# Performance work log

Measured on AMD Instinct MI355X. Metric: run time of the kernel, lower is better.

Reference implementation:

```python
import jax, jax.numpy as jnp
import numpy as np

B, I, P, H = 256, 1024, 128, 128
L_PROT = 1024
ATOMS_PER_MOL = 128
N_LIG = B * ATOMS_PER_MOL  # 32768 total ligand atoms


def setup_inputs() -> dict:
    key = jax.random.key(0)
    ks = jax.random.split(key, 6)
    param_enc = jax.random.normal(ks[0], (B, I, P), dtype=jnp.float32)
    h_prot = jax.random.normal(ks[1], (B, L_PROT, H), dtype=jnp.float32)
    w1 = jax.random.normal(ks[2], (P, 1), dtype=jnp.float32) / np.sqrt(P)
    b1 = jax.random.normal(ks[3], (1,), dtype=jnp.float32)
    indices_lig = jax.random.randint(ks[4], (B, I), 0, ATOMS_PER_MOL)
    indices_prot = jax.random.randint(ks[5], (B, I), 0, L_PROT)
    protein_idx = jnp.arange(B)            # complex b -> protein row b
    lig_offsets = jnp.arange(B) * ATOMS_PER_MOL  # 'split' cumulative atom offsets
    mask = jnp.ones((B, I), dtype=bool)    # valid (non -510 padded) interactions
    return {
        "param_enc": param_enc, "h_prot": h_prot, "w1": w1, "b1": b1,
        "indices_lig": indices_lig, "indices_prot": indices_prot,
        "protein_idx": protein_idx, "lig_offsets": lig_offsets, "mask": mask,
    }


def reference(param_enc, h_prot, w1, b1, indices_lig, indices_prot,
              protein_idx, lig_offsets, mask):
    # scalar gate per interaction: ReLU(Linear(param_enc))  (dropout = identity, eval mode)
    gate = jax.nn.relu(jnp.einsum("bip,po->bio", param_enc, w1) + b1)  # [B, I, 1]
    # gather protein residue features: h_prot[protein_idx[b], indices_prot[b,i], :]
    gathered = h_prot[protein_idx[:, None], indices_prot]              # [B, I, H]
    contrib = gate * gathered * mask[..., None]                        # [B, I, H]
    # scatter-add into per-ligand-atom accumulator at split + i_l
    glob = (lig_offsets[:, None] + indices_lig).reshape(-1)            # [B*I]
    protein_inter = jnp.zeros((N_LIG, H), dtype=contrib.dtype)
    protein_inter = protein_inter.at[glob].add(contrib.reshape(-1, H))
    return protein_inter
```

## Files before the change

kernel.cpp:

```cpp
#include <hip/hip_runtime.h>

#define B_ 256
#define I_ 1024
#define P_ 128
#define H_ 128
#define LP_ 1024

__global__ __launch_bounds__(256) void gates_gemv(
    const float* __restrict__ param_enc,
    const float* __restrict__ w1,
    const float* __restrict__ b1,
    float* __restrict__ gates)
{
    const int tid  = threadIdx.x;
    const int lane = tid & 63;
    const int wave = tid >> 6;
    const int half = lane >> 5;
    const int sub  = lane & 31;
    const int w    = blockIdx.x * 4 + wave;
    const int b    = w >> 5;
    const int wwb  = w & 31;

    const float bias = b1[0];
    const float4 wv = *(const float4*)(w1 + sub * 4);
    const float* pe_b = param_enc + (size_t)b * I_ * P_;
    float* g_b = gates + b * I_;

    #pragma unroll 8
    for (int q = 0; q < 16; ++q) {
        const int i0 = (wwb + q * 32) * 2;
        float4 pv = *(const float4*)(pe_b + (size_t)i0 * P_ + lane * 4);
        float part = pv.x * wv.x + pv.y * wv.y + pv.z * wv.z + pv.w * wv.w;
        part += __shfl_xor(part, 1);
        part += __shfl_xor(part, 2);
        part += __shfl_xor(part, 4);
        part += __shfl_xor(part, 8);
        part += __shfl_xor(part, 16);
        if (sub == 0) g_b[i0 + half] = part + bias;
    }
}

__global__ __launch_bounds__(256) void sort_gather(
    const float* __restrict__ gates,
    const float* __restrict__ h_prot,
    const int* __restrict__ indices_lig,
    const int* __restrict__ indices_prot,
    const int* __restrict__ protein_idx,
    const int* __restrict__ lig_offsets,
    float* __restrict__ out)
{
    __shared__ float          s_g[I_];
    __shared__ unsigned short s_ipl[I_];
    __shared__ unsigned short s_items[I_];
    __shared__ int            s_cnt[32];
    __shared__ int            s_start[33];
    __shared__ int            s_cur[32];

    const int tid  = threadIdx.x;
    const int blk  = blockIdx.x;
    const int b    = blk >> 2;
    const int rseg = (blk & 3) << 5;
    const int lane = tid & 63;
    const int wave = tid >> 6;
    const int half = lane >> 5;
    const int sub  = lane & 31;
    const int halfIdx = wave * 2 + half;

    if (tid < 32) s_cnt[tid] = 0;

    const int pb = protein_idx[b];
    const float* hp_b = h_prot + (size_t)pb * LP_ * H_;
    const float* g_b  = gates + b * I_;
    const int* il_b   = indices_lig + b * I_;
    const int* ip_b   = indices_prot + b * I_;

    __syncthreads();

    int  rloc[4];
    bool lv[4];
    #pragma unroll
    for (int k = 0; k < 4; ++k) {
        const int i  = tid + k * 256;
        const float g = g_b[i];
        const int il  = il_b[i];
        const int ip  = ip_b[i];
        s_g[i]   = g;
        s_ipl[i] = (unsigned short)ip;
        const int r = il - rseg;
        lv[k]   = (g > 0.f) && ((unsigned)r < 32u);
        rloc[k] = r;
        if (lv[k]) atomicAdd(&s_cnt[r], 1);
    }
    __syncthreads();

    if (wave == 0) {
        const int c = (lane < 32) ? s_cnt[lane] : 0;
        int s = c;
        #pragma unroll
        for (int d = 1; d < 32; d <<= 1) {
            const int t = __shfl_up(s, d);
            if (lane >= d) s += t;
        }
        if (lane < 32) { s_start[lane] = s - c; s_cur[lane] = s - c; }
        if (lane == 31) s_start[32] = s;
    }
    __syncthreads();

    #pragma unroll
    for (int k = 0; k < 4; ++k) {
        if (lv[k]) {
            const int pos = atomicAdd(&s_cur[rloc[k]], 1);
            s_items[pos] = (unsigned short)(tid + k * 256);
        }
    }
    __syncthreads();

    int st[4], cn[4];
    #pragma unroll
    for (int rr = 0; rr < 4; ++rr) {
        const int a = halfIdx + rr * 8;
        st[rr] = s_start[a];
        cn[rr] = s_start[a + 1] - st[rr];
    }
    float4 acc[4];
    #pragma unroll
    for (int rr = 0; rr < 4; ++rr) acc[rr] = make_float4(0.f, 0.f, 0.f, 0.f);

    const int mx = max(max(cn[0], cn[1]), max(cn[2], cn[3]));
    for (int j = 0; j < mx; ++j) {
        #pragma unroll
        for (int rr = 0; rr < 4; ++rr) {
            if (j < cn[rr]) {
                const int   item = s_items[st[rr] + j];
                const float g    = s_g[item];
                const int   ip   = s_ipl[item];
                const float4 hv  = *(const float4*)(hp_b + (size_t)ip * H_ + sub * 4);
                acc[rr].x += g * hv.x;
                acc[rr].y += g * hv.y;
                acc[rr].z += g * hv.z;
                acc[rr].w += g * hv.w;
            }
        }
    }

    const int base = lig_offsets[b] + rseg;
    #pragma unroll
    for (int rr = 0; rr < 4; ++rr) {
        float* o = out + (size_t)(base + halfIdx + rr * 8) * H_;
        *(float4*)(o + sub * 4) = acc[rr];
    }
}

__global__ __launch_bounds__(1024) void fused_ile(
    const float* __restrict__ param_enc,
    const float* __restrict__ h_prot,
    const float* __restrict__ w1,
    const float* __restrict__ b1,
    const int* __restrict__ indices_lig,
    const int* __restrict__ indices_prot,
    const int* __restrict__ protein_idx,
    const int* __restrict__ lig_offsets,
    float* __restrict__ out)
{
    __shared__ float          s_gate[I_];
    __shared__ unsigned short s_ip[I_];
    __shared__ unsigned short s_items[I_];
    __shared__ int            s_cnt[128];
    __shared__ int            s_start[129];
    __shared__ int            s_cur[128];

    const int tid  = threadIdx.x;
    const int b    = blockIdx.x;
    const int lane = tid & 63;
    const int wave = tid >> 6;
    const int half = lane >> 5;
    const int sub  = lane & 31;
    const int halfIdx = wave * 2 + half;

    if (tid < 128) s_cnt[tid] = 0;

    const float bias = b1[0];
    const int pb = protein_idx[b];
    const float4 wv = *(const float4*)(w1 + sub * 4);

    const float* pe_b = param_enc + (size_t)b * I_ * P_;
    const float* hp_b = h_prot + (size_t)pb * LP_ * H_;
    const int* il_b = indices_lig + b * I_;
    const int* ip_b = indices_prot + b * I_;

    #pragma unroll 8
    for (int q = 0; q < 32; ++q) {
        const int p  = wave + q * 16;
        const int i0 = p * 2;
        float4 pv = *(const float4*)(pe_b + (size_t)i0 * P_ + lane * 4);
        float part = pv.x * wv.x + pv.y * wv.y + pv.z * wv.z + pv.w * wv.w;
        part += __shfl_xor(part, 1);
        part += __shfl_xor(part, 2);
        part += __shfl_xor(part, 4);
        part += __shfl_xor(part, 8);
        part += __shfl_xor(part, 16);
        if (sub == 0) s_gate[i0 + half] = part + bias;
    }
    __syncthreads();

    const int  my_il = il_b[tid];
    const int  my_ip = ip_b[tid];
    const bool live  = s_gate[tid] > 0.f;
    s_ip[tid] = (unsigned short)my_ip;
    if (live) atomicAdd(&s_cnt[my_il], 1);
    __syncthreads();

    if (wave == 0) {
        const int c0 = s_cnt[2 * lane];
        const int c1 = s_cnt[2 * lane + 1];
        int s = c0 + c1;
        #pragma unroll
        for (int d = 1; d < 64; d <<= 1) {
            int t = __shfl_up(s, d);
            if (lane >= d) s += t;
        }
        s_start[2 * lane]     = s - c0 - c1;
        s_start[2 * lane + 1] = s - c1;
        if (lane == 63) s_start[128] = s;
    }
    __syncthreads();
    if (tid < 128) s_cur[tid] = s_start[tid];
    __syncthreads();

    if (live) {
        const int pos = atomicAdd(&s_cur[my_il], 1);
        s_items[pos] = (unsigned short)tid;
    }
    __syncthreads();

    const int base = lig_offsets[b];
    int st[4], cn[4];
    #pragma unroll
    for (int rr = 0; rr < 4; ++rr) {
        const int a = halfIdx + rr * 32;
        st[rr] = s_start[a];
        cn[rr] = s_start[a + 1] - st[rr];
    }
    float4 acc[4];
    #pragma unroll
    for (int rr = 0; rr < 4; ++rr) acc[rr] = make_float4(0.f, 0.f, 0.f, 0.f);

    int mx = max(max(cn[0], cn[1]), max(cn[2], cn[3]));
    for (int j = 0; j < mx; ++j) {
        #pragma unroll
        for (int rr = 0; rr < 4; ++rr) {
            if (j < cn[rr]) {
                const int   item = s_items[st[rr] + j];
                const float g    = s_gate[item];
                const int   ip   = s_ip[item];
                const float4 hv  = *(const float4*)(hp_b + (size_t)ip * H_ + sub * 4);
                acc[rr].x += g * hv.x;
                acc[rr].y += g * hv.y;
                acc[rr].z += g * hv.z;
                acc[rr].w += g * hv.w;
            }
        }
    }

    #pragma unroll
    for (int rr = 0; rr < 4; ++rr) {
        float* o = out + (size_t)(base + halfIdx + rr * 32) * H_;
        *(float4*)(o + sub * 4) = acc[rr];
    }
}

extern "C" void kernel_launch(void* const* d_in, const int* in_sizes, int n_in,
                              void* d_out, int out_size, void* d_ws, size_t ws_size,
                              hipStream_t stream) {
    const float* param_enc   = (const float*)d_in[0];
    const float* h_prot      = (const float*)d_in[1];
    const float* w1          = (const float*)d_in[2];
    const float* b1          = (const float*)d_in[3];
    const int* indices_lig   = (const int*)d_in[4];
    const int* indices_prot  = (const int*)d_in[5];
    const int* protein_idx   = (const int*)d_in[6];
    const int* lig_offsets   = (const int*)d_in[7];
    float* out = (float*)d_out;

    const size_t gates_bytes = (size_t)B_ * I_ * sizeof(float);
    if (ws_size >= gates_bytes && d_ws != nullptr) {
        float* gates = (float*)d_ws;
        gates_gemv<<<B_ * 8, 256, 0, stream>>>(param_enc, w1, b1, gates);
        sort_gather<<<B_ * 4, 256, 0, stream>>>(gates, h_prot,
                                                indices_lig, indices_prot,
                                                protein_idx, lig_offsets, out);
    } else {
        fused_ile<<<B_, 1024, 0, stream>>>(param_enc, h_prot, w1, b1,
                                           indices_lig, indices_prot,
                                           protein_idx, lig_offsets, out);
    }
}
```

Baseline: 283.9 us.

## Remap gate GEMV to 8-lane rows and split scatter-gather into 16-row segments

The gate GEMV now gives each group of 8 lanes a full 128-wide row, loaded as four float4 chunks per lane. This cuts the shuffle reduction from 5 steps to 3 and makes each wave cover contiguous rows. The sort-gather kernel now splits each complex into 8 segments of 16 ligand atoms instead of 4 segments of 32, which doubles the block count and halves the accumulators per thread. The aim is more parallelism and fewer registers in the gather phase. In exchange, each block re-reads all 1024 gates and indices for its complex, so that redundant index and gate traffic doubles.

```diff
diff --git a/kernel.cpp b/kernel.cpp
--- a/kernel.cpp
+++ b/kernel.cpp
@@ -15,28 +15,37 @@
     const int tid  = threadIdx.x;
     const int lane = tid & 63;
     const int wave = tid >> 6;
-    const int half = lane >> 5;
-    const int sub  = lane & 31;
     const int w    = blockIdx.x * 4 + wave;
     const int b    = w >> 5;
     const int wwb  = w & 31;
+    const int row8 = lane >> 3;
+    const int oct  = lane & 7;
 
     const float bias = b1[0];
-    const float4 wv = *(const float4*)(w1 + sub * 4);
+    const float4 wl0 = *(const float4*)(w1 + oct * 4);
+    const float4 wl1 = *(const float4*)(w1 + 32 + oct * 4);
+    const float4 wl2 = *(const float4*)(w1 + 64 + oct * 4);
+    const float4 wl3 = *(const float4*)(w1 + 96 + oct * 4);
+
     const float* pe_b = param_enc + (size_t)b * I_ * P_;
     float* g_b = gates + b * I_;
 
-    #pragma unroll 8
-    for (int q = 0; q < 16; ++q) {
-        const int i0 = (wwb + q * 32) * 2;
-        float4 pv = *(const float4*)(pe_b + (size_t)i0 * P_ + lane * 4);
-        float part = pv.x * wv.x + pv.y * wv.y + pv.z * wv.z + pv.w * wv.w;
-        part += __shfl_xor(part, 1);
-        part += __shfl_xor(part, 2);
-        part += __shfl_xor(part, 4);
-        part += __shfl_xor(part, 8);
-        part += __shfl_xor(part, 16);
-        if (sub == 0) g_b[i0 + half] = part + bias;
+    #pragma unroll 2
+    for (int q = 0; q < 4; ++q) {
+        const int i0 = wwb * 32 + q * 8;
+        const float* base = pe_b + (size_t)(i0 + row8) * P_ + oct * 4;
+        const float4 a0 = *(const float4*)(base);
+        const float4 a1 = *(const float4*)(base + 32);
+        const float4 a2 = *(const float4*)(base + 64);
+        const float4 a3 = *(const float4*)(base + 96);
+        float s = a0.x * wl0.x + a0.y * wl0.y + a0.z * wl0.z + a0.w * wl0.w
+                + a1.x * wl1.x + a1.y * wl1.y + a1.z * wl1.z + a1.w * wl1.w
+                + a2.x * wl2.x + a2.y * wl2.y + a2.z * wl2.z + a2.w * wl2.w
+                + a3.x * wl3.x + a3.y * wl3.y + a3.z * wl3.z + a3.w * wl3.w;
+        s += __shfl_xor(s, 1);
+        s += __shfl_xor(s, 2);
+        s += __shfl_xor(s, 4);
+        if (oct == 0) g_b[i0 + row8] = s + bias;
     }
 }
 
@@ -52,21 +61,21 @@
     __shared__ float          s_g[I_];
     __shared__ unsigned short s_ipl[I_];
     __shared__ unsigned short s_items[I_];
-    __shared__ int            s_cnt[32];
-    __shared__ int            s_start[33];
-    __shared__ int            s_cur[32];
+    __shared__ int            s_cnt[16];
+    __shared__ int            s_start[17];
+    __shared__ int            s_cur[16];
 
     const int tid  = threadIdx.x;
     const int blk  = blockIdx.x;
-    const int b    = blk >> 2;
-    const int rseg = (blk & 3) << 5;
+    const int b    = blk >> 3;
+    const int rseg = (blk & 7) << 4;
     const int lane = tid & 63;
     const int wave = tid >> 6;
     const int half = lane >> 5;
     const int sub  = lane & 31;
     const int halfIdx = wave * 2 + half;
 
-    if (tid < 32) s_cnt[tid] = 0;
+    if (tid < 16) s_cnt[tid] = 0;
 
     const int pb = protein_idx[b];
     const float* hp_b = h_prot + (size_t)pb * LP_ * H_;
@@ -80,29 +89,29 @@
     bool lv[4];
     #pragma unroll
     for (int k = 0; k < 4; ++k) {
-        const int i  = tid + k * 256;
+        const int i   = tid + k * 256;
         const float g = g_b[i];
         const int il  = il_b[i];
         const int ip  = ip_b[i];
         s_g[i]   = g;
         s_ipl[i] = (unsigned short)ip;
         const int r = il - rseg;
-        lv[k]   = (g > 0.f) && ((unsigned)r < 32u);
+        lv[k]   = (g > 0.f) && ((unsigned)r < 16u);
         rloc[k] = r;
         if (lv[k]) atomicAdd(&s_cnt[r], 1);
     }
     __syncthreads();
 
     if (wave == 0) {
-        const int c = (lane < 32) ? s_cnt[lane] : 0;
+        const int c = (lane < 16) ? s_cnt[lane] : 0;
         int s = c;
         #pragma unroll
-        for (int d = 1; d < 32; d <<= 1) {
+        for (int d = 1; d < 16; d <<= 1) {
             const int t = __shfl_up(s, d);
             if (lane >= d) s += t;
         }
-        if (lane < 32) { s_start[lane] = s - c; s_cur[lane] = s - c; }
-        if (lane == 31) s_start[32] = s;
+        if (lane < 16) { s_start[lane] = s - c; s_cur[lane] = s - c; }
+        if (lane == 15) s_start[16] = s;
     }
     __syncthreads();
 
@@ -115,40 +124,39 @@
     }
     __syncthreads();
 
-    int st[4], cn[4];
-    #pragma unroll
-    for (int rr = 0; rr < 4; ++rr) {
-        const int a = halfIdx + rr * 8;
-        st[rr] = s_start[a];
-        cn[rr] = s_start[a + 1] - st[rr];
-    }
-    float4 acc[4];
-    #pragma unroll
-    for (int rr = 0; rr < 4; ++rr) acc[rr] = make_float4(0.f, 0.f, 0.f, 0.f);
-
-    const int mx = max(max(cn[0], cn[1]), max(cn[2], cn[3]));
+    const int st0 = s_start[halfIdx];
+    const int cn0 = s_start[halfIdx + 1] - st0;
+    const int st1 = s_start[halfIdx + 8];
+    const int cn1 = s_start[halfIdx + 9] - st1;
+    float4 a0 = make_float4(0.f, 0.f, 0.f, 0.f);
+    float4 a1 = make_float4(0.f, 0.f, 0.f, 0.f);
+
+    const int mx = max(cn0, cn1);
+    #pragma unroll 2
     for (int j = 0; j < mx; ++j) {
-        #pragma unroll
-        for (int rr = 0; rr < 4; ++rr) {
-            if (j < cn[rr]) {
-                const int   item = s_items[st[rr] + j];
-                const float g    = s_g[item];
-                const int   ip   = s_ipl[item];
-                const float4 hv  = *(const float4*)(hp_b + (size_t)ip * H_ + sub * 4);
-                acc[rr].x += g * hv.x;
-                acc[rr].y += g * hv.y;
-                acc[rr].z += g * hv.z;
-                acc[rr].w += g * hv.w;
-            }
+        if (j < cn0) {
+            const int   item = s_items[st0 + j];
+            const float g    = s_g[item];
+            const int   ip   = s_ipl[item];
+            const float4 hv  = *(const float4*)(hp_b + (size_t)ip * H_ + sub * 4);
+            a0.x += g * hv.x; a0.y += g * hv.y;
+            a0.z += g * hv.z; a0.w += g * hv.w;
+        }
+        if (j < cn1) {
+            const int   item = s_items[st1 + j];
+            const float g    = s_g[item];
+            const int   ip   = s_ipl[item];
+            const float4 hv  = *(const float4*)(hp_b + (size_t)ip * H_ + sub * 4);
+            a1.x += g * hv.x; a1.y += g * hv.y;
+            a1.z += g * hv.z; a1.w += g * hv.w;
         }
     }
 
     const int base = lig_offsets[b] + rseg;
-    #pragma unroll
-    for (int rr = 0; rr < 4; ++rr) {
-        float* o = out + (size_t)(base + halfIdx + rr * 8) * H_;
-        *(float4*)(o + sub * 4) = acc[rr];
-    }
+    float* o0 = out + (size_t)(base + halfIdx) * H_;
+    float* o1 = out + (size_t)(base + halfIdx + 8) * H_;
+    *(float4*)(o0 + sub * 4) = a0;
+    *(float4*)(o1 + sub * 4) = a1;
 }
 
 __global__ __launch_bounds__(1024) void fused_ile(
@@ -285,10 +293,10 @@
     const size_t gates_bytes = (size_t)B_ * I_ * sizeof(float);
     if (ws_size >= gates_bytes && d_ws != nullptr) {
         float* gates = (float*)d_ws;
-        gates_gemv<<<B_ * 8, 256, 0, stream>>>(param_enc, w1, b1, gates);
-        sort_gather<<<B_ * 4, 256, 0, stream>>>(gates, h_prot,
-                                                indices_lig, indices_prot,
-                                                protein_idx, lig_offsets, out);
+        gates_gemv<<<2048, 256, 0, stream>>>(param_enc, w1, b1, gates);
+        sort_gather<<<2048, 256, 0, stream>>>(gates, h_prot,
+                                              indices_lig, indices_prot,
+                                              protein_idx, lig_offsets, out);
     } else {
         fused_ile<<<B_, 1024, 0, stream>>>(param_enc, h_prot, w1, b1,
                                            indices_lig, indices_prot,
```

Measured after the change: 278.1 us. -2.1%, faster.
